# Kernel optimization log

Hardware: AMD Instinct MI355X
Metric: run time of the kernel (lower is better)

## Reference

```python
import jax, jax.numpy as jnp
import numpy as np

NUM_HEADS = 12
HEAD_DIM = 64
HIDDEN = 768
QMAX = 127.0  # 8-bit symmetric
DOMAIN_MIN, DOMAIN_MAX = -10.0, 0.0
NUM_INTERVALS = 12


def _build_pla_coeffs():
    xs = np.linspace(DOMAIN_MIN, DOMAIN_MAX, 1001)
    ys = np.exp(xs)
    intervals = np.linspace(DOMAIN_MIN, DOMAIN_MAX, NUM_INTERVALS + 1)
    ms, cs = [], []
    for i in range(NUM_INTERVALS):
        a, b = intervals[i], intervals[i + 1]
        mask = (xs >= a) & (xs <= b)
        m, c = np.polyfit(xs[mask], ys[mask], 1)
        ms.append(m)
        cs.append(c)
    return (jnp.asarray(ms, jnp.float32), jnp.asarray(cs, jnp.float32),
            jnp.asarray(intervals, jnp.float32))

COEFFS_M, COEFFS_C, INTERVALS = _build_pla_coeffs()


def quantize(x):
    # per-row (last-dim) abs-max symmetric 8-bit fake quant
    max_val = jnp.max(jnp.abs(x), axis=-1, keepdims=True)
    scale = max_val / QMAX
    scale = jnp.where(scale == 0, 1.0, scale)
    return jnp.clip(jnp.round(x / scale), -QMAX, QMAX) * scale


def to_fixed_point(x, bits=32, frac_bits=26):
    scale = 2.0 ** frac_bits
    lo = -2.0 ** (bits - 1)
    hi = 2.0 ** (bits - 1) - 1
    return jnp.clip(jnp.round(x * scale), lo, hi) / scale


def pla_exp(x):
    xc = jnp.clip(x, DOMAIN_MIN, DOMAIN_MAX)
    # sum(x >= intervals) - 1 == searchsorted(intervals, x, 'right') - 1
    idx = jnp.clip(jnp.searchsorted(INTERVALS, xc, side='right') - 1, 0, NUM_INTERVALS - 1)
    return COEFFS_M[idx] * xc + COEFFS_C[idx]


def pla_softmax(scores):
    shifted = scores - jnp.max(scores, axis=-1, keepdims=True)
    shifted_fx = to_fixed_point(shifted, 32, 26)
    exps = pla_exp(shifted_fx)
    sm = exps / (jnp.sum(exps, axis=-1, keepdims=True) + 1e-9)
    return quantize(sm)


def q_linear(x, W, b):
    # QuantizedLinear: quantize input and weight (per-row), fp bias
    return quantize(x) @ quantize(W).T + b


def split_heads(x):
    B, S, _ = x.shape
    return x.reshape(B, S, NUM_HEADS, HEAD_DIM).transpose(0, 2, 1, 3)  # bhsd


def mhsa(hidden_states, Wq, bq, Wk, bk, Wv, bv, Wo, bo):
    B, S, H = hidden_states.shape
    scale = HEAD_DIM ** -0.5
    q = split_heads(q_linear(hidden_states, Wq, bq))
    k = split_heads(q_linear(hidden_states, Wk, bk))
    v = split_heads(q_linear(hidden_states, Wv, bv))
    # per-row quantization makes tile-wise quant identical to full quant
    scores = jnp.einsum('bhqd,bhkd->bhqk', quantize(q), quantize(k)) * scale
    probs = pla_softmax(scores)
    ctx = jnp.einsum('bhqk,bhkd->bhqd', probs, quantize(v))
    ctx = ctx.transpose(0, 2, 1, 3).reshape(B, S, H)
    return q_linear(ctx, Wo, bo)


def setup_inputs() -> dict:
    key = jax.random.key(0)
    ks = jax.random.split(key, 9)
    B, S = 8, 512
    hs = jax.random.normal(ks[0], (B, S, HIDDEN), dtype=jnp.float32)
    def w(k):
        return jax.random.normal(k, (HIDDEN, HIDDEN), dtype=jnp.float32) * 0.02
    def b(k):
        return jax.random.normal(k, (HIDDEN,), dtype=jnp.float32) * 0.02
    return {
        'hidden_states': hs,
        'Wq': w(ks[1]), 'bq': b(ks[2]),
        'Wk': w(ks[3]), 'bk': b(ks[4]),
        'Wv': w(ks[5]), 'bv': b(ks[6]),
        'Wo': w(ks[7]), 'bo': b(ks[8]),
    }


def reference(hidden_states, Wq, bq, Wk, bk, Wv, bv, Wo, bo):
    return mhsa(hidden_states, Wq, bq, Wk, bk, Wv, bv, Wo, bo)
```

## Files before the change

kernel.cpp:

```cpp
#include <hip/hip_runtime.h>
#include <cmath>

#define R_TOT 4096
#define HID   768
#define NHEAD 12
#define HDIM  64
#define SEQ   512
#define BATCH 8

typedef int   v4i  __attribute__((ext_vector_type(4)));
typedef float v4f  __attribute__((ext_vector_type(4)));
typedef _Float16 half8 __attribute__((ext_vector_type(8)));
typedef _Float16 half4v __attribute__((ext_vector_type(4)));

struct PlaConsts { float m[12]; float c[12]; float b[13]; };

static PlaConsts build_pla() {
  PlaConsts pc;
  const int NPTS = 1001;
  static double xs[NPTS], ys[NPTS];
  const double step = 10.0 / 1000.0;
  for (int j = 0; j < NPTS; ++j) xs[j] = (double)j * step + (-10.0);
  xs[NPTS - 1] = 0.0;
  for (int j = 0; j < NPTS; ++j) ys[j] = std::exp(xs[j]);
  double bnd[13];
  const double step2 = 10.0 / 12.0;
  for (int k = 0; k < 13; ++k) bnd[k] = (double)k * step2 + (-10.0);
  bnd[12] = 0.0;
  for (int i = 0; i < 12; ++i) {
    const double a = bnd[i], bb = bnd[i + 1];
    double sx = 0, sy = 0; int n = 0;
    for (int j = 0; j < NPTS; ++j)
      if (xs[j] >= a && xs[j] <= bb) { sx += xs[j]; sy += ys[j]; ++n; }
    const double xm = sx / n, ym = sy / n;
    double sxx = 0, sxy = 0;
    for (int j = 0; j < NPTS; ++j)
      if (xs[j] >= a && xs[j] <= bb) {
        const double dx = xs[j] - xm;
        sxx += dx * dx; sxy += dx * (ys[j] - ym);
      }
    const double m = sxy / sxx;
    pc.m[i] = (float)m;
    pc.c[i] = (float)(ym - m * xm);
  }
  for (int k = 0; k < 13; ++k) pc.b[k] = (float)bnd[k];
  return pc;
}
static const PlaConsts g_pla = build_pla();

__device__ __forceinline__ void quant_row_body(const float* __restrict__ x,
                                               signed char* __restrict__ qrow,
                                               float* __restrict__ srow,
                                               int ncols) {
  float m = 0.f;
  for (int c = threadIdx.x; c < ncols; c += 256)
    m = fmaxf(m, fabsf(x[c]));
  #pragma unroll
  for (int off = 32; off; off >>= 1) m = fmaxf(m, __shfl_xor(m, off));
  __shared__ float red[4];
  const int lane = threadIdx.x & 63, wv = threadIdx.x >> 6;
  if (lane == 0) red[wv] = m;
  __syncthreads();
  if (threadIdx.x == 0) {
    float mm = fmaxf(fmaxf(red[0], red[1]), fmaxf(red[2], red[3]));
    float s = mm / 127.0f;
    if (s == 0.f) s = 1.f;
    red[0] = s;
    *srow = s;
  }
  __syncthreads();
  const float s = red[0];
  for (int c = threadIdx.x; c < ncols; c += 256) {
    float q = rintf(x[c] / s);
    q = fminf(fmaxf(q, -127.f), 127.f);
    qrow[c] = (signed char)(int)q;
  }
}

__global__ __launch_bounds__(256)
void quant_rows(const float* __restrict__ src, int ncols,
                signed char* __restrict__ qout, float* __restrict__ sout) {
  const int row = blockIdx.x;
  quant_row_body(src + (size_t)row * ncols, qout + (size_t)row * ncols,
                 sout + row, ncols);
}

__global__ __launch_bounds__(256)
void quant_w4(const float* w0, const float* w1, const float* w2, const float* w3,
              signed char* q0, signed char* q1, signed char* q2, signed char* q3,
              float* s0, float* s1, float* s2, float* s3) {
  const int row = blockIdx.x;
  const float* src; signed char* qo; float* so;
  switch (blockIdx.y) {
    case 0: src = w0; qo = q0; so = s0; break;
    case 1: src = w1; qo = q1; so = s1; break;
    case 2: src = w2; qo = q2; so = s2; break;
    default: src = w3; qo = q3; so = s3; break;
  }
  quant_row_body(src + (size_t)row * HID, qo + (size_t)row * HID, so + row, HID);
}

template <int MODE>
__global__ __launch_bounds__(256)
void proj_mfma(const signed char* __restrict__ qx, const float* __restrict__ sx,
               const signed char* __restrict__ qw, const float* __restrict__ sw,
               const float* __restrict__ bias,
               signed char* __restrict__ qo, float* __restrict__ so,
               _Float16* __restrict__ vt, float* __restrict__ fo) {
  __shared__ __align__(16) signed char Al[64 * 80];
  __shared__ __align__(16) signed char Bl[64 * 80];
  const int tid = threadIdx.x;
  const int w = tid >> 6, lane = tid & 63;
  const int n = lane & 15, quad = lane >> 4;
  const int row0 = blockIdx.x * 64, col0 = blockIdx.y * 64;
  const int lr = tid >> 2, seg = tid & 3;
  v4i acc[4];
  #pragma unroll
  for (int j = 0; j < 4; ++j) acc[j] = (v4i){0, 0, 0, 0};
  for (int k0 = 0; k0 < HID; k0 += 64) {
    const int4 av = *(const int4*)(qx + (size_t)(row0 + lr) * HID + k0 + seg * 16);
    const int4 bv = *(const int4*)(qw + (size_t)(col0 + lr) * HID + k0 + seg * 16);
    if (k0) __syncthreads();
    *(int4*)&Al[lr * 80 + seg * 16] = av;
    *(int4*)&Bl[lr * 80 + seg * 16] = bv;
    __syncthreads();
    const v4i af = *(const v4i*)&Al[(w * 16 + n) * 80 + quad * 16];
    #pragma unroll
    for (int j = 0; j < 4; ++j) {
      const v4i bf = *(const v4i*)&Bl[(j * 16 + n) * 80 + quad * 16];
      acc[j] = __builtin_amdgcn_mfma_i32_16x16x64_i8(af, bf, acc[j], 0, 0, 0);
    }
  }
  const int mrow = w * 16 + quad * 4;
  float sxr[4];
  #pragma unroll
  for (int r = 0; r < 4; ++r) sxr[r] = sx[row0 + mrow + r];
  float vals[4][4];
  #pragma unroll
  for (int j = 0; j < 4; ++j) {
    const float swc = sw[col0 + j * 16 + n];
    const float bc = bias[col0 + j * 16 + n];
    #pragma unroll
    for (int r = 0; r < 4; ++r)
      vals[j][r] = (float)acc[j][r] * (sxr[r] * swc) + bc;
  }
  if (MODE == 1) {
    const int h = blockIdx.y;
    #pragma unroll
    for (int r = 0; r < 4; ++r) {
      float m = 0.f;
      #pragma unroll
      for (int j = 0; j < 4; ++j) m = fmaxf(m, fabsf(vals[j][r]));
      #pragma unroll
      for (int off = 1; off < 16; off <<= 1) m = fmaxf(m, __shfl_xor(m, off));
      float s = m / 127.0f;
      if (s == 0.f) s = 1.f;
      const int grow = row0 + mrow + r;
      const int bidx = grow >> 9, sidx = grow & 511;
      const size_t rowidx = ((size_t)bidx * NHEAD + h) * SEQ + sidx;
      #pragma unroll
      for (int j = 0; j < 4; ++j) {
        float q = fminf(fmaxf(rintf(vals[j][r] / s), -127.f), 127.f);
        qo[rowidx * HDIM + j * 16 + n] = (signed char)(int)q;
      }
      if (n == 0) so[rowidx] = s;
    }
  } else if (MODE == 2) {
    const int h = blockIdx.y;
    float srow[4];
    #pragma unroll
    for (int r = 0; r < 4; ++r) {
      float m = 0.f;
      #pragma unroll
      for (int j = 0; j < 4; ++j) m = fmaxf(m, fabsf(vals[j][r]));
      #pragma unroll
      for (int off = 1; off < 16; off <<= 1) m = fmaxf(m, __shfl_xor(m, off));
      float s = m / 127.0f;
      if (s == 0.f) s = 1.f;
      srow[r] = s;
    }
    const int grow0 = row0 + mrow;
    const int bidx = grow0 >> 9, sidx = grow0 & 511;
    const size_t hbv = (size_t)bidx * NHEAD + h;
    #pragma unroll
    for (int j = 0; j < 4; ++j) {
      half4v hv;
      #pragma unroll
      for (int r = 0; r < 4; ++r) {
        float q = fminf(fmaxf(rintf(vals[j][r] / srow[r]), -127.f), 127.f);
        hv[r] = (_Float16)(q * srow[r]);
      }
      *(half4v*)(vt + (hbv * HDIM + j * 16 + n) * SEQ + sidx) = hv;
    }
  } else {
    #pragma unroll
    for (int r = 0; r < 4; ++r) {
      const size_t base = (size_t)(row0 + mrow + r) * HID + col0;
      #pragma unroll
      for (int j = 0; j < 4; ++j)
        fo[base + j * 16 + n] = vals[j][r];
    }
  }
}

#define PSTR 520
__global__ __launch_bounds__(256)
void attn_kernel(const signed char* __restrict__ qq, const float* __restrict__ qss,
                 const signed char* __restrict__ qk, const float* __restrict__ kss,
                 const _Float16* __restrict__ vth,
                 float* __restrict__ ctx, const PlaConsts pc) {
  __shared__ __align__(16) _Float16 PhT[16 * PSTR];
  __shared__ __align__(16) float red_max[16][4], red_sum[16][4], red_amax[16][4];
  __shared__ float psa[16];
  __shared__ __align__(8) float pb2[12][2];
  __shared__ __align__(8) float pmc[12][2];

  const int tid = threadIdx.x;
  const int q0 = blockIdx.x * 16;
  const int hh = blockIdx.y, bz = blockIdx.z;
  const size_t hb = (size_t)bz * NHEAD + hh;
  const signed char* qqh = qq + (hb * SEQ + q0) * HDIM;
  const signed char* qkh = qk + hb * SEQ * HDIM;
  const float* ksp = kss + hb * SEQ;

  if (tid < 12) {
    pb2[tid][0] = pc.b[tid]; pb2[tid][1] = pc.b[tid + 1];
    pmc[tid][0] = pc.m[tid]; pmc[tid][1] = pc.c[tid];
  }

  const int w = tid >> 6, lane = tid & 63;
  const int n = lane & 15, quad = lane >> 4;

  float s26[8][4];
  {
    const v4i qfrag = *(const v4i*)(qqh + (size_t)n * HDIM + quad * 16);
    const float qs26 = (qss[hb * SEQ + q0 + n] * 0.125f) * 67108864.0f;
    float vmax = -3.0e38f;
    #pragma unroll
    for (int t = 0; t < 8; ++t) {
      const int kc0 = (t * 4 + w) * 16;
      const v4i kfrag = *(const v4i*)(qkh + (size_t)(kc0 + n) * HDIM + quad * 16);
      const float4 ks4 = *(const float4*)(ksp + kc0 + quad * 4);
      v4i zero = {};
      const v4i acc = __builtin_amdgcn_mfma_i32_16x16x64_i8(kfrag, qfrag, zero, 0, 0, 0);
      const float ks[4] = {ks4.x, ks4.y, ks4.z, ks4.w};
      #pragma unroll
      for (int r = 0; r < 4; ++r) {
        const float v = (float)acc[r] * (qs26 * ks[r]);
        s26[t][r] = v;
        vmax = fmaxf(vmax, v);
      }
    }
    vmax = fmaxf(vmax, __shfl_xor(vmax, 16));
    vmax = fmaxf(vmax, __shfl_xor(vmax, 32));
    if (quad == 0) red_max[n][w] = vmax;
  }
  __syncthreads();

  {
    const float4 rm = *(const float4*)&red_max[n][0];
    const float mx26 = fmaxf(fmaxf(rm.x, rm.y), fmaxf(rm.z, rm.w));
    float sum = 0.f, amax = 0.f;
    #pragma unroll
    for (int t = 0; t < 8; ++t) {
      #pragma unroll
      for (int r = 0; r < 4; ++r) {
        float sh = s26[t][r] - mx26;
        sh = fmaxf(sh, -671088640.0f);
        const float tq = rintf(sh);
        const float xc = tq * 1.4901161193847656e-08f;
        int g = (int)floorf((xc + 10.0f) * 1.2f);
        g = g < 0 ? 0 : (g > 11 ? 11 : g);
        const float2 bb = *(const float2*)&pb2[g][0];
        if (xc < bb.x) --g;
        else if (xc >= bb.y) ++g;
        g = g < 0 ? 0 : (g > 11 ? 11 : g);
        const float2 mc = *(const float2*)&pmc[g][0];
        const float e = __fadd_rn(__fmul_rn(mc.x, xc), mc.y);
        s26[t][r] = e;
        sum += e;
        amax = fmaxf(amax, fabsf(e));
      }
    }
    sum += __shfl_xor(sum, 16);
    sum += __shfl_xor(sum, 32);
    amax = fmaxf(amax, __shfl_xor(amax, 16));
    amax = fmaxf(amax, __shfl_xor(amax, 32));
    if (quad == 0) { red_sum[n][w] = sum; red_amax[n][w] = amax; }
    __syncthreads();
    const float4 rs = *(const float4*)&red_sum[n][0];
    const float4 ra = *(const float4*)&red_amax[n][0];
    float denom = (rs.x + rs.y) + (rs.z + rs.w);
    denom = __fadd_rn(denom, 1e-9f);
    const float rden = 1.0f / denom;
    const float am = fmaxf(fmaxf(ra.x, ra.y), fmaxf(ra.z, ra.w));
    float ps = (am * rden) / 127.0f;
    if (ps == 0.f) ps = 1.f;
    const float rps = 1.0f / ps;
    if (w == 0 && quad == 0) psa[n] = ps;
    #pragma unroll
    for (int t = 0; t < 8; ++t) {
      half4v hq;
      #pragma unroll
      for (int r = 0; r < 4; ++r) {
        const float p = s26[t][r] * rden;
        const float qf = fminf(fmaxf(rintf(p * rps), -127.f), 127.f);
        hq[r] = (_Float16)qf;
      }
      *(half4v*)&PhT[n * PSTR + (t * 4 + w) * 16 + quad * 4] = hq;
    }
  }
  __syncthreads();

  {
    v4f accf = {0.f, 0.f, 0.f, 0.f};
    const _Float16* vrow = vth + ((size_t)hb * HDIM + w * 16 + n) * SEQ + quad * 8;
    const _Float16* prow = &PhT[n * PSTR + quad * 8];
    #pragma unroll 4
    for (int kt = 0; kt < 16; ++kt) {
      const half8 bf = *(const half8*)(vrow + kt * 32);
      const half8 af = *(const half8*)(prow + kt * 32);
      accf = __builtin_amdgcn_mfma_f32_16x16x32_f16(af, bf, accf, 0, 0, 0);
    }
    #pragma unroll
    for (int r = 0; r < 4; ++r) {
      const int row = quad * 4 + r;
      const float o = accf[r] * psa[row];
      ctx[((size_t)bz * SEQ + q0 + row) * HID + (size_t)hh * HDIM + w * 16 + n] = o;
    }
  }
}

extern "C" void kernel_launch(void* const* d_in, const int* in_sizes, int n_in,
                              void* d_out, int out_size, void* d_ws, size_t ws_size,
                              hipStream_t stream) {
  (void)in_sizes; (void)n_in; (void)out_size; (void)ws_size;
  const float* hs = (const float*)d_in[0];
  const float* Wq = (const float*)d_in[1];
  const float* bq = (const float*)d_in[2];
  const float* Wk = (const float*)d_in[3];
  const float* bk = (const float*)d_in[4];
  const float* Wv = (const float*)d_in[5];
  const float* bv = (const float*)d_in[6];
  const float* Wo = (const float*)d_in[7];
  const float* bo = (const float*)d_in[8];
  float* out = (float*)d_out;

  char* ws = (char*)d_ws;
  size_t off = 0;
  auto alloc = [&](size_t bytes) -> char* {
    char* p = ws + off;
    off += (bytes + 255) & ~(size_t)255;
    return p;
  };
  signed char* qx  = (signed char*)alloc((size_t)R_TOT * HID);
  float*       sx  = (float*)alloc((size_t)R_TOT * 4);
  signed char* qwq = (signed char*)alloc((size_t)HID * HID);
  signed char* qwk = (signed char*)alloc((size_t)HID * HID);
  signed char* qwv = (signed char*)alloc((size_t)HID * HID);
  signed char* qwo = (signed char*)alloc((size_t)HID * HID);
  float*       swq = (float*)alloc((size_t)HID * 4);
  float*       swk = (float*)alloc((size_t)HID * 4);
  float*       swv = (float*)alloc((size_t)HID * 4);
  float*       swo = (float*)alloc((size_t)HID * 4);
  signed char* qqd = (signed char*)alloc((size_t)R_TOT * HID);
  float*       qqs = (float*)alloc((size_t)BATCH * NHEAD * SEQ * 4);
  signed char* qkd = (signed char*)alloc((size_t)R_TOT * HID);
  float*       qks = (float*)alloc((size_t)BATCH * NHEAD * SEQ * 4);
  float*       ctx = (float*)alloc((size_t)R_TOT * HID * 4);
  _Float16*    vth = (_Float16*)alloc((size_t)BATCH * NHEAD * HDIM * SEQ * 2);
  signed char* qc  = qx;
  float*       scs = sx;

  quant_rows<<<R_TOT, 256, 0, stream>>>(hs, HID, qx, sx);
  quant_w4<<<dim3(HID, 4), 256, 0, stream>>>(Wq, Wk, Wv, Wo,
                                             qwq, qwk, qwv, qwo,
                                             swq, swk, swv, swo);

  const dim3 pg(R_TOT / 64, HID / 64);
  proj_mfma<1><<<pg, 256, 0, stream>>>(qx, sx, qwq, swq, bq, qqd, qqs, nullptr, nullptr);
  proj_mfma<1><<<pg, 256, 0, stream>>>(qx, sx, qwk, swk, bk, qkd, qks, nullptr, nullptr);
  proj_mfma<2><<<pg, 256, 0, stream>>>(qx, sx, qwv, swv, bv, nullptr, nullptr, vth, nullptr);

  attn_kernel<<<dim3(SEQ / 16, NHEAD, BATCH), 256, 0, stream>>>(
      qqd, qqs, qkd, qks, vth, ctx, g_pla);

  quant_rows<<<R_TOT, 256, 0, stream>>>(ctx, HID, qc, scs);
  proj_mfma<0><<<pg, 256, 0, stream>>>(qc, scs, qwo, swo, bo, nullptr, nullptr, nullptr, out);
}
```

Baseline: 179.7 us.

## Fuse QKV projections, enlarge GEMM and attention tiles, and block V layout

The three Q/K/V projection launches become one grid with a z dimension. Projection tiles grow from 64 to 128 rows so each loaded weight fragment feeds two MFMAs. The attention kernel now handles 32 queries per block, reusing K fragments and V loads across two query groups. V is stored in a blocked layout of 32-key chunks so PV loads are contiguous. This cuts launch count and redundant global loads, at the cost of fewer blocks, more registers per thread and more LDS for attention.

```diff
diff --git a/kernel.cpp b/kernel.cpp
--- a/kernel.cpp
+++ b/kernel.cpp
@@ -100,123 +100,165 @@
   quant_row_body(src + (size_t)row * HID, qo + (size_t)row * HID, so + row, HID);
 }
 
-template <int MODE>
-__global__ __launch_bounds__(256)
-void proj_mfma(const signed char* __restrict__ qx, const float* __restrict__ sx,
+__device__ __forceinline__
+void proj_body(int mode,
+               const signed char* __restrict__ qx, const float* __restrict__ sx,
                const signed char* __restrict__ qw, const float* __restrict__ sw,
                const float* __restrict__ bias,
                signed char* __restrict__ qo, float* __restrict__ so,
-               _Float16* __restrict__ vt, float* __restrict__ fo) {
-  __shared__ __align__(16) signed char Al[64 * 80];
-  __shared__ __align__(16) signed char Bl[64 * 80];
+               _Float16* __restrict__ vt, float* __restrict__ fo,
+               signed char* Al, signed char* Bl) {
   const int tid = threadIdx.x;
   const int w = tid >> 6, lane = tid & 63;
   const int n = lane & 15, quad = lane >> 4;
-  const int row0 = blockIdx.x * 64, col0 = blockIdx.y * 64;
-  const int lr = tid >> 2, seg = tid & 3;
-  v4i acc[4];
-  #pragma unroll
-  for (int j = 0; j < 4; ++j) acc[j] = (v4i){0, 0, 0, 0};
+  const int row0 = blockIdx.x * 128, col0 = blockIdx.y * 64;
+  const int ar = tid >> 1, aseg = (tid & 1) * 32;
+  const int br = tid >> 2, bseg = (tid & 3) * 16;
+  v4i acc[2][4];
+  #pragma unroll
+  for (int s = 0; s < 2; ++s)
+    #pragma unroll
+    for (int j = 0; j < 4; ++j) acc[s][j] = (v4i){0, 0, 0, 0};
   for (int k0 = 0; k0 < HID; k0 += 64) {
-    const int4 av = *(const int4*)(qx + (size_t)(row0 + lr) * HID + k0 + seg * 16);
-    const int4 bv = *(const int4*)(qw + (size_t)(col0 + lr) * HID + k0 + seg * 16);
+    const int4 a0 = *(const int4*)(qx + (size_t)(row0 + ar) * HID + k0 + aseg);
+    const int4 a1 = *(const int4*)(qx + (size_t)(row0 + ar) * HID + k0 + aseg + 16);
+    const int4 b0 = *(const int4*)(qw + (size_t)(col0 + br) * HID + k0 + bseg);
     if (k0) __syncthreads();
-    *(int4*)&Al[lr * 80 + seg * 16] = av;
-    *(int4*)&Bl[lr * 80 + seg * 16] = bv;
+    *(int4*)&Al[ar * 80 + aseg] = a0;
+    *(int4*)&Al[ar * 80 + aseg + 16] = a1;
+    *(int4*)&Bl[br * 80 + bseg] = b0;
     __syncthreads();
-    const v4i af = *(const v4i*)&Al[(w * 16 + n) * 80 + quad * 16];
+    const v4i af0 = *(const v4i*)&Al[(w * 16 + n) * 80 + quad * 16];
+    const v4i af1 = *(const v4i*)&Al[(64 + w * 16 + n) * 80 + quad * 16];
     #pragma unroll
     for (int j = 0; j < 4; ++j) {
       const v4i bf = *(const v4i*)&Bl[(j * 16 + n) * 80 + quad * 16];
-      acc[j] = __builtin_amdgcn_mfma_i32_16x16x64_i8(af, bf, acc[j], 0, 0, 0);
-    }
-  }
-  const int mrow = w * 16 + quad * 4;
-  float sxr[4];
-  #pragma unroll
-  for (int r = 0; r < 4; ++r) sxr[r] = sx[row0 + mrow + r];
-  float vals[4][4];
+      acc[0][j] = __builtin_amdgcn_mfma_i32_16x16x64_i8(af0, bf, acc[0][j], 0, 0, 0);
+      acc[1][j] = __builtin_amdgcn_mfma_i32_16x16x64_i8(af1, bf, acc[1][j], 0, 0, 0);
+    }
+  }
+  float swc4[4], bc4[4];
   #pragma unroll
   for (int j = 0; j < 4; ++j) {
-    const float swc = sw[col0 + j * 16 + n];
-    const float bc = bias[col0 + j * 16 + n];
-    #pragma unroll
-    for (int r = 0; r < 4; ++r)
-      vals[j][r] = (float)acc[j][r] * (sxr[r] * swc) + bc;
-  }
-  if (MODE == 1) {
-    const int h = blockIdx.y;
-    #pragma unroll
-    for (int r = 0; r < 4; ++r) {
-      float m = 0.f;
-      #pragma unroll
-      for (int j = 0; j < 4; ++j) m = fmaxf(m, fabsf(vals[j][r]));
-      #pragma unroll
-      for (int off = 1; off < 16; off <<= 1) m = fmaxf(m, __shfl_xor(m, off));
-      float s = m / 127.0f;
-      if (s == 0.f) s = 1.f;
-      const int grow = row0 + mrow + r;
-      const int bidx = grow >> 9, sidx = grow & 511;
-      const size_t rowidx = ((size_t)bidx * NHEAD + h) * SEQ + sidx;
+    swc4[j] = sw[col0 + j * 16 + n];
+    bc4[j] = bias[col0 + j * 16 + n];
+  }
+  #pragma unroll
+  for (int s = 0; s < 2; ++s) {
+    const int mrow = s * 64 + w * 16 + quad * 4;
+    float sxr[4];
+    #pragma unroll
+    for (int r = 0; r < 4; ++r) sxr[r] = sx[row0 + mrow + r];
+    float vals[4][4];
+    #pragma unroll
+    for (int j = 0; j < 4; ++j)
+      #pragma unroll
+      for (int r = 0; r < 4; ++r)
+        vals[j][r] = (float)acc[s][j][r] * (sxr[r] * swc4[j]) + bc4[j];
+    if (mode == 1) {
+      const int h = blockIdx.y;
+      #pragma unroll
+      for (int r = 0; r < 4; ++r) {
+        float m = 0.f;
+        #pragma unroll
+        for (int j = 0; j < 4; ++j) m = fmaxf(m, fabsf(vals[j][r]));
+        #pragma unroll
+        for (int off = 1; off < 16; off <<= 1) m = fmaxf(m, __shfl_xor(m, off));
+        float sq = m / 127.0f;
+        if (sq == 0.f) sq = 1.f;
+        const int grow = row0 + mrow + r;
+        const int bidx = grow >> 9, sidx = grow & 511;
+        const size_t rowidx = ((size_t)bidx * NHEAD + h) * SEQ + sidx;
+        #pragma unroll
+        for (int j = 0; j < 4; ++j) {
+          float q = fminf(fmaxf(rintf(vals[j][r] / sq), -127.f), 127.f);
+          qo[rowidx * HDIM + j * 16 + n] = (signed char)(int)q;
+        }
+        if (n == 0) so[rowidx] = sq;
+      }
+    } else if (mode == 2) {
+      const int h = blockIdx.y;
+      float srow[4];
+      #pragma unroll
+      for (int r = 0; r < 4; ++r) {
+        float m = 0.f;
+        #pragma unroll
+        for (int j = 0; j < 4; ++j) m = fmaxf(m, fabsf(vals[j][r]));
+        #pragma unroll
+        for (int off = 1; off < 16; off <<= 1) m = fmaxf(m, __shfl_xor(m, off));
+        float sq = m / 127.0f;
+        if (sq == 0.f) sq = 1.f;
+        srow[r] = sq;
+      }
+      const int grow0 = row0 + mrow;
+      const int bidx = grow0 >> 9, sidx = grow0 & 511;
+      const int kb = sidx >> 5, ko = sidx & 31;
+      const size_t hbv = (size_t)bidx * NHEAD + h;
       #pragma unroll
       for (int j = 0; j < 4; ++j) {
-        float q = fminf(fmaxf(rintf(vals[j][r] / s), -127.f), 127.f);
-        qo[rowidx * HDIM + j * 16 + n] = (signed char)(int)q;
-      }
-      if (n == 0) so[rowidx] = s;
-    }
-  } else if (MODE == 2) {
-    const int h = blockIdx.y;
-    float srow[4];
-    #pragma unroll
-    for (int r = 0; r < 4; ++r) {
-      float m = 0.f;
-      #pragma unroll
-      for (int j = 0; j < 4; ++j) m = fmaxf(m, fabsf(vals[j][r]));
-      #pragma unroll
-      for (int off = 1; off < 16; off <<= 1) m = fmaxf(m, __shfl_xor(m, off));
-      float s = m / 127.0f;
-      if (s == 0.f) s = 1.f;
-      srow[r] = s;
-    }
-    const int grow0 = row0 + mrow;
-    const int bidx = grow0 >> 9, sidx = grow0 & 511;
-    const size_t hbv = (size_t)bidx * NHEAD + h;
-    #pragma unroll
-    for (int j = 0; j < 4; ++j) {
-      half4v hv;
-      #pragma unroll
-      for (int r = 0; r < 4; ++r) {
-        float q = fminf(fmaxf(rintf(vals[j][r] / srow[r]), -127.f), 127.f);
-        hv[r] = (_Float16)(q * srow[r]);
-      }
-      *(half4v*)(vt + (hbv * HDIM + j * 16 + n) * SEQ + sidx) = hv;
-    }
-  } else {
-    #pragma unroll
-    for (int r = 0; r < 4; ++r) {
-      const size_t base = (size_t)(row0 + mrow + r) * HID + col0;
-      #pragma unroll
-      for (int j = 0; j < 4; ++j)
-        fo[base + j * 16 + n] = vals[j][r];
-    }
-  }
+        half4v hv;
+        #pragma unroll
+        for (int r = 0; r < 4; ++r) {
+          float q = fminf(fmaxf(rintf(vals[j][r] / srow[r]), -127.f), 127.f);
+          hv[r] = (_Float16)(q * srow[r]);
+        }
+        *(half4v*)(vt + ((hbv * 16 + kb) * 64 + j * 16 + n) * 32 + ko) = hv;
+      }
+    } else {
+      #pragma unroll
+      for (int r = 0; r < 4; ++r) {
+        const size_t base = (size_t)(row0 + mrow + r) * HID + col0;
+        #pragma unroll
+        for (int j = 0; j < 4; ++j)
+          fo[base + j * 16 + n] = vals[j][r];
+      }
+    }
+  }
+}
+
+__global__ __launch_bounds__(256)
+void proj_qkv(const signed char* __restrict__ qx, const float* __restrict__ sx,
+              const signed char* qwq, const float* swq, const float* bq,
+              signed char* qqd, float* qqs,
+              const signed char* qwk, const float* swk, const float* bk,
+              signed char* qkd, float* qks,
+              const signed char* qwv, const float* swv, const float* bv,
+              _Float16* vt2) {
+  __shared__ __align__(16) signed char Al[128 * 80];
+  __shared__ __align__(16) signed char Bl[64 * 80];
+  if (blockIdx.z == 0)
+    proj_body(1, qx, sx, qwq, swq, bq, qqd, qqs, nullptr, nullptr, Al, Bl);
+  else if (blockIdx.z == 1)
+    proj_body(1, qx, sx, qwk, swk, bk, qkd, qks, nullptr, nullptr, Al, Bl);
+  else
+    proj_body(2, qx, sx, qwv, swv, bv, nullptr, nullptr, vt2, nullptr, Al, Bl);
+}
+
+__global__ __launch_bounds__(256)
+void proj_out(const signed char* __restrict__ qx, const float* __restrict__ sx,
+              const signed char* qw, const float* sw, const float* bias,
+              float* fo) {
+  __shared__ __align__(16) signed char Al[128 * 80];
+  __shared__ __align__(16) signed char Bl[64 * 80];
+  proj_body(0, qx, sx, qw, sw, bias, nullptr, nullptr, nullptr, fo, Al, Bl);
 }
 
 #define PSTR 520
 __global__ __launch_bounds__(256)
 void attn_kernel(const signed char* __restrict__ qq, const float* __restrict__ qss,
                  const signed char* __restrict__ qk, const float* __restrict__ kss,
-                 const _Float16* __restrict__ vth,
+                 const _Float16* __restrict__ vt2,
                  float* __restrict__ ctx, const PlaConsts pc) {
-  __shared__ __align__(16) _Float16 PhT[16 * PSTR];
-  __shared__ __align__(16) float red_max[16][4], red_sum[16][4], red_amax[16][4];
-  __shared__ float psa[16];
+  __shared__ __align__(16) _Float16 PhT[2 * 16 * PSTR];
+  __shared__ __align__(16) float red_max[2][16][4];
+  __shared__ __align__(16) float red_sum[2][16][4];
+  __shared__ __align__(16) float red_amax[2][16][4];
+  __shared__ float psa[2][16];
   __shared__ __align__(8) float pb2[12][2];
   __shared__ __align__(8) float pmc[12][2];
 
   const int tid = threadIdx.x;
-  const int q0 = blockIdx.x * 16;
+  const int q0 = blockIdx.x * 32;
   const int hh = blockIdx.y, bz = blockIdx.z;
   const size_t hb = (size_t)bz * NHEAD + hh;
   const signed char* qqh = qq + (hb * SEQ + q0) * HDIM;
@@ -231,41 +273,48 @@
   const int w = tid >> 6, lane = tid & 63;
   const int n = lane & 15, quad = lane >> 4;
 
-  float s26[8][4];
+  float s26[2][8][4];
   {
-    const v4i qfrag = *(const v4i*)(qqh + (size_t)n * HDIM + quad * 16);
-    const float qs26 = (qss[hb * SEQ + q0 + n] * 0.125f) * 67108864.0f;
-    float vmax = -3.0e38f;
+    const v4i qf0 = *(const v4i*)(qqh + (size_t)n * HDIM + quad * 16);
+    const v4i qf1 = *(const v4i*)(qqh + (size_t)(16 + n) * HDIM + quad * 16);
+    const float qs0 = (qss[hb * SEQ + q0 + n] * 0.125f) * 67108864.0f;
+    const float qs1 = (qss[hb * SEQ + q0 + 16 + n] * 0.125f) * 67108864.0f;
+    float vmax0 = -3.0e38f, vmax1 = -3.0e38f;
     #pragma unroll
     for (int t = 0; t < 8; ++t) {
       const int kc0 = (t * 4 + w) * 16;
       const v4i kfrag = *(const v4i*)(qkh + (size_t)(kc0 + n) * HDIM + quad * 16);
       const float4 ks4 = *(const float4*)(ksp + kc0 + quad * 4);
       v4i zero = {};
-      const v4i acc = __builtin_amdgcn_mfma_i32_16x16x64_i8(kfrag, qfrag, zero, 0, 0, 0);
+      const v4i a0 = __builtin_amdgcn_mfma_i32_16x16x64_i8(kfrag, qf0, zero, 0, 0, 0);
+      const v4i a1 = __builtin_amdgcn_mfma_i32_16x16x64_i8(kfrag, qf1, zero, 0, 0, 0);
       const float ks[4] = {ks4.x, ks4.y, ks4.z, ks4.w};
       #pragma unroll
       for (int r = 0; r < 4; ++r) {
-        const float v = (float)acc[r] * (qs26 * ks[r]);
-        s26[t][r] = v;
-        vmax = fmaxf(vmax, v);
-      }
-    }
-    vmax = fmaxf(vmax, __shfl_xor(vmax, 16));
-    vmax = fmaxf(vmax, __shfl_xor(vmax, 32));
-    if (quad == 0) red_max[n][w] = vmax;
+        const float v0 = (float)a0[r] * (qs0 * ks[r]);
+        const float v1 = (float)a1[r] * (qs1 * ks[r]);
+        s26[0][t][r] = v0; vmax0 = fmaxf(vmax0, v0);
+        s26[1][t][r] = v1; vmax1 = fmaxf(vmax1, v1);
+      }
+    }
+    vmax0 = fmaxf(vmax0, __shfl_xor(vmax0, 16));
+    vmax0 = fmaxf(vmax0, __shfl_xor(vmax0, 32));
+    vmax1 = fmaxf(vmax1, __shfl_xor(vmax1, 16));
+    vmax1 = fmaxf(vmax1, __shfl_xor(vmax1, 32));
+    if (quad == 0) { red_max[0][n][w] = vmax0; red_max[1][n][w] = vmax1; }
   }
   __syncthreads();
 
-  {
-    const float4 rm = *(const float4*)&red_max[n][0];
+  #pragma unroll
+  for (int tau = 0; tau < 2; ++tau) {
+    const float4 rm = *(const float4*)&red_max[tau][n][0];
     const float mx26 = fmaxf(fmaxf(rm.x, rm.y), fmaxf(rm.z, rm.w));
     float sum = 0.f, amax = 0.f;
     #pragma unroll
     for (int t = 0; t < 8; ++t) {
       #pragma unroll
       for (int r = 0; r < 4; ++r) {
-        float sh = s26[t][r] - mx26;
+        float sh = s26[tau][t][r] - mx26;
         sh = fmaxf(sh, -671088640.0f);
         const float tq = rintf(sh);
         const float xc = tq * 1.4901161193847656e-08f;
@@ -277,7 +326,7 @@
         g = g < 0 ? 0 : (g > 11 ? 11 : g);
         const float2 mc = *(const float2*)&pmc[g][0];
         const float e = __fadd_rn(__fmul_rn(mc.x, xc), mc.y);
-        s26[t][r] = e;
+        s26[tau][t][r] = e;
         sum += e;
         amax = fmaxf(amax, fabsf(e));
       }
@@ -286,10 +335,14 @@
     sum += __shfl_xor(sum, 32);
     amax = fmaxf(amax, __shfl_xor(amax, 16));
     amax = fmaxf(amax, __shfl_xor(amax, 32));
-    if (quad == 0) { red_sum[n][w] = sum; red_amax[n][w] = amax; }
-    __syncthreads();
-    const float4 rs = *(const float4*)&red_sum[n][0];
-    const float4 ra = *(const float4*)&red_amax[n][0];
+    if (quad == 0) { red_sum[tau][n][w] = sum; red_amax[tau][n][w] = amax; }
+  }
+  __syncthreads();
+
+  #pragma unroll
+  for (int tau = 0; tau < 2; ++tau) {
+    const float4 rs = *(const float4*)&red_sum[tau][n][0];
+    const float4 ra = *(const float4*)&red_amax[tau][n][0];
     float denom = (rs.x + rs.y) + (rs.z + rs.w);
     denom = __fadd_rn(denom, 1e-9f);
     const float rden = 1.0f / denom;
@@ -297,36 +350,38 @@
     float ps = (am * rden) / 127.0f;
     if (ps == 0.f) ps = 1.f;
     const float rps = 1.0f / ps;
-    if (w == 0 && quad == 0) psa[n] = ps;
+    if (w == 0 && quad == 0) psa[tau][n] = ps;
     #pragma unroll
     for (int t = 0; t < 8; ++t) {
       half4v hq;
       #pragma unroll
       for (int r = 0; r < 4; ++r) {
-        const float p = s26[t][r] * rden;
+        const float p = s26[tau][t][r] * rden;
         const float qf = fminf(fmaxf(rintf(p * rps), -127.f), 127.f);
         hq[r] = (_Float16)qf;
       }
-      *(half4v*)&PhT[n * PSTR + (t * 4 + w) * 16 + quad * 4] = hq;
+      *(half4v*)&PhT[(tau * 16 + n) * PSTR + (t * 4 + w) * 16 + quad * 4] = hq;
     }
   }
   __syncthreads();
 
   {
-    v4f accf = {0.f, 0.f, 0.f, 0.f};
-    const _Float16* vrow = vth + ((size_t)hb * HDIM + w * 16 + n) * SEQ + quad * 8;
-    const _Float16* prow = &PhT[n * PSTR + quad * 8];
+    v4f acc0 = {0.f, 0.f, 0.f, 0.f}, acc1 = {0.f, 0.f, 0.f, 0.f};
+    const _Float16* vbase = vt2 + ((size_t)hb * 16 * 64 + (w * 16 + n)) * 32 + quad * 8;
+    const _Float16* p0 = &PhT[n * PSTR + quad * 8];
+    const _Float16* p1 = &PhT[(16 + n) * PSTR + quad * 8];
     #pragma unroll 4
     for (int kt = 0; kt < 16; ++kt) {
-      const half8 bf = *(const half8*)(vrow + kt * 32);
-      const half8 af = *(const half8*)(prow + kt * 32);
-      accf = __builtin_amdgcn_mfma_f32_16x16x32_f16(af, bf, accf, 0, 0, 0);
+      const half8 bf = *(const half8*)(vbase + kt * 2048);
+      acc0 = __builtin_amdgcn_mfma_f32_16x16x32_f16(*(const half8*)(p0 + kt * 32), bf, acc0, 0, 0, 0);
+      acc1 = __builtin_amdgcn_mfma_f32_16x16x32_f16(*(const half8*)(p1 + kt * 32), bf, acc1, 0, 0, 0);
     }
     #pragma unroll
     for (int r = 0; r < 4; ++r) {
       const int row = quad * 4 + r;
-      const float o = accf[r] * psa[row];
-      ctx[((size_t)bz * SEQ + q0 + row) * HID + (size_t)hh * HDIM + w * 16 + n] = o;
+      const size_t cbase = (size_t)hh * HDIM + w * 16 + n;
+      ctx[((size_t)bz * SEQ + q0 + row) * HID + cbase] = acc0[r] * psa[0][row];
+      ctx[((size_t)bz * SEQ + q0 + 16 + row) * HID + cbase] = acc1[r] * psa[1][row];
     }
   }
 }
@@ -368,7 +423,7 @@
   signed char* qkd = (signed char*)alloc((size_t)R_TOT * HID);
   float*       qks = (float*)alloc((size_t)BATCH * NHEAD * SEQ * 4);
   float*       ctx = (float*)alloc((size_t)R_TOT * HID * 4);
-  _Float16*    vth = (_Float16*)alloc((size_t)BATCH * NHEAD * HDIM * SEQ * 2);
+  _Float16*    vt2 = (_Float16*)alloc((size_t)BATCH * NHEAD * HDIM * SEQ * 2);
   signed char* qc  = qx;
   float*       scs = sx;
 
@@ -377,14 +432,15 @@
                                              qwq, qwk, qwv, qwo,
                                              swq, swk, swv, swo);
 
-  const dim3 pg(R_TOT / 64, HID / 64);
-  proj_mfma<1><<<pg, 256, 0, stream>>>(qx, sx, qwq, swq, bq, qqd, qqs, nullptr, nullptr);
-  proj_mfma<1><<<pg, 256, 0, stream>>>(qx, sx, qwk, swk, bk, qkd, qks, nullptr, nullptr);
-  proj_mfma<2><<<pg, 256, 0, stream>>>(qx, sx, qwv, swv, bv, nullptr, nullptr, vth, nullptr);
-
-  attn_kernel<<<dim3(SEQ / 16, NHEAD, BATCH), 256, 0, stream>>>(
-      qqd, qqs, qkd, qks, vth, ctx, g_pla);
+  proj_qkv<<<dim3(R_TOT / 128, HID / 64, 3), 256, 0, stream>>>(
+      qx, sx, qwq, swq, bq, qqd, qqs,
+      qwk, swk, bk, qkd, qks,
+      qwv, swv, bv, vt2);
+
+  attn_kernel<<<dim3(SEQ / 32, NHEAD, BATCH), 256, 0, stream>>>(
+      qqd, qqs, qkd, qks, vt2, ctx, g_pla);
 
   quant_rows<<<R_TOT, 256, 0, stream>>>(ctx, HID, qc, scs);
-  proj_mfma<0><<<pg, 256, 0, stream>>>(qc, scs, qwo, swo, bo, nullptr, nullptr, nullptr, out);
-}
+  proj_out<<<dim3(R_TOT / 128, HID / 64), 256, 0, stream>>>(
+      qc, scs, qwo, swo, bo, out);
+}
```

After: 166.1 us. 7.6% less time.
